# Performance work log

Measured on AMD Instinct MI355X. Metric: run time of the kernel, lower is better.

Reference implementation:

```python
import jax, jax.numpy as jnp
import numpy as np

B, S, D, H, FF = 4, 2048, 512, 8, 2048
HD = D // H
WINDOW = 64  # local attention half-window in rank space
EPS = 1e-5


def _layer_norm(v, g, b):
    m = jnp.mean(v, axis=-1, keepdims=True)
    var = jnp.mean(jnp.square(v - m), axis=-1, keepdims=True)
    return (v - m) / jnp.sqrt(var + EPS) * g + b


def setup_inputs() -> dict:
    key = jax.random.key(0)
    ks = jax.random.split(key, 10)
    sc = 0.02
    x = jax.random.normal(ks[0], (B, S, D), jnp.float32)
    padding_mask = jnp.zeros((B, S), dtype=bool)
    i = jnp.arange(S)
    local = jnp.abs(i[:, None] - i[None, :]) <= WINDOW
    glob = (i[:, None] == 0) | (i[None, :] == 0)  # global spectrum token at pos 0
    attn_mask = jnp.where(local | glob, 0.0, -jnp.inf).astype(jnp.float32)
    return {
        "x": x,
        "padding_mask": padding_mask,
        "attn_mask": attn_mask,
        "in_proj_w": jax.random.normal(ks[1], (3 * D, D), jnp.float32) * sc,
        "in_proj_b": jnp.zeros((3 * D,), jnp.float32),
        "out_proj_w": jax.random.normal(ks[2], (D, D), jnp.float32) * sc,
        "out_proj_b": jnp.zeros((D,), jnp.float32),
        "ln1_g": jnp.ones((D,), jnp.float32),
        "ln1_b": jnp.zeros((D,), jnp.float32),
        "ln2_g": jnp.ones((D,), jnp.float32),
        "ln2_b": jnp.zeros((D,), jnp.float32),
        "ff_w1": jax.random.normal(ks[3], (FF, D), jnp.float32) * sc,
        "ff_b1": jnp.zeros((FF,), jnp.float32),
        "ff_w2": jax.random.normal(ks[4], (D, FF), jnp.float32) * sc,
        "ff_b2": jnp.zeros((D,), jnp.float32),
    }


def reference(x, padding_mask, attn_mask, in_proj_w, in_proj_b, out_proj_w,
              out_proj_b, ln1_g, ln1_b, ln2_g, ln2_b, ff_w1, ff_b1, ff_w2, ff_b2):
    # pre-LN attention
    a = _layer_norm(x, ln1_g, ln1_b)
    qkv = a @ in_proj_w.T + in_proj_b  # [B,S,3D]
    q, k, v = jnp.split(qkv, 3, axis=-1)
    to_heads = lambda t: t.reshape(B, S, H, HD).transpose(0, 2, 1, 3)
    q, k, v = to_heads(q), to_heads(k), to_heads(v)
    scores = jnp.einsum('bhqd,bhkd->bhqk', q, k) * (HD ** -0.5)
    # float attn_mask path: key_padding_mask converted to additive -inf floats
    kpm = jnp.where(padding_mask, -jnp.inf, 0.0).astype(scores.dtype)
    scores = scores + attn_mask[None, None, :, :] + kpm[:, None, None, :]
    p = jax.nn.softmax(scores, axis=-1)
    o = jnp.einsum('bhqk,bhkd->bhqd', p, v).transpose(0, 2, 1, 3).reshape(B, S, D)
    o = o @ out_proj_w.T + out_proj_b
    x = x + o  # residual (dropout = 0)
    # pre-LN feed-forward with exact GELU (torch nn.GELU default)
    f = _layer_norm(x, ln2_g, ln2_b)
    f = jax.nn.gelu(f @ ff_w1.T + ff_b1, approximate=False) @ ff_w2.T + ff_b2
    return x + f
```

## Files before the change

### kernel.cpp

```cpp
#include <hip/hip_runtime.h>
#include <hip/hip_bf16.h>
#include <math.h>

namespace {

constexpr int kB = 4, kS = 2048, kD = 512, kH = 8, kFF = 2048;
constexpr int kM = kB * kS;
constexpr int kHD = kD / kH;
constexpr int kWin = 64;

typedef __attribute__((ext_vector_type(8))) short short8;
typedef __attribute__((ext_vector_type(4))) float f32x4;

__device__ __forceinline__ float bf2f(__hip_bfloat16 v) { return __bfloat162float(v); }
__device__ __forceinline__ __hip_bfloat16 f2bf(float v) { return __float2bfloat16(v); }
__device__ __forceinline__ int iclamp(int v, int lo, int hi) { return v < lo ? lo : (v > hi ? hi : v); }

__device__ __forceinline__ void async16(const void* g, void* l) {
  __builtin_amdgcn_global_load_lds((const __attribute__((address_space(1))) void*)g,
                                   (__attribute__((address_space(3))) void*)l, 16, 0, 0);
}

__device__ __forceinline__ void ln_one_row_f32(const float* xr, const float* g,
                                               const float* bta, __hip_bfloat16* outr, int lane) {
  int c = lane * 8;
  float4 v0 = *(const float4*)(xr + c);
  float4 v1 = *(const float4*)(xr + c + 4);
  float s  = v0.x + v0.y + v0.z + v0.w + v1.x + v1.y + v1.z + v1.w;
  float ss = v0.x*v0.x + v0.y*v0.y + v0.z*v0.z + v0.w*v0.w
           + v1.x*v1.x + v1.y*v1.y + v1.z*v1.z + v1.w*v1.w;
#pragma unroll
  for (int o = 32; o > 0; o >>= 1) { s += __shfl_xor(s, o); ss += __shfl_xor(ss, o); }
  float mean = s * (1.0f / kD);
  float inv  = rsqrtf(ss * (1.0f / kD) - mean * mean + 1e-5f);
  float4 g0 = *(const float4*)(g + c),   g1 = *(const float4*)(g + c + 4);
  float4 b0 = *(const float4*)(bta + c), b1 = *(const float4*)(bta + c + 4);
  union { __hip_bfloat16 h[8]; int4 u; } t;
  t.h[0] = f2bf((v0.x - mean) * inv * g0.x + b0.x);
  t.h[1] = f2bf((v0.y - mean) * inv * g0.y + b0.y);
  t.h[2] = f2bf((v0.z - mean) * inv * g0.z + b0.z);
  t.h[3] = f2bf((v0.w - mean) * inv * g0.w + b0.w);
  t.h[4] = f2bf((v1.x - mean) * inv * g1.x + b1.x);
  t.h[5] = f2bf((v1.y - mean) * inv * g1.y + b1.y);
  t.h[6] = f2bf((v1.z - mean) * inv * g1.z + b1.z);
  t.h[7] = f2bf((v1.w - mean) * inv * g1.w + b1.w);
  *(int4*)(outr + c) = t.u;
}

__global__ __launch_bounds__(256)
void prep(const float* __restrict__ iw, const float* __restrict__ ow,
          const float* __restrict__ f1, const float* __restrict__ f2,
          __hip_bfloat16* __restrict__ wq, __hip_bfloat16* __restrict__ wo,
          __hip_bfloat16* __restrict__ w1, __hip_bfloat16* __restrict__ w2,
          const float* __restrict__ x, const float* __restrict__ g,
          const float* __restrict__ bta, __hip_bfloat16* __restrict__ a) {
  const int id = blockIdx.x;
  if (id < 3072) {
    const float* s; __hip_bfloat16* d; int base;
    if (id < 768)       { s = iw; d = wq; base = id; }
    else if (id < 1024) { s = ow; d = wo; base = id - 768; }
    else if (id < 2048) { s = f1; d = w1; base = id - 1024; }
    else                { s = f2; d = w2; base = id - 2048; }
    int i = base * 1024 + threadIdx.x * 4;
    float4 v = *(const float4*)(s + i);
    union { __hip_bfloat16 h[4]; uint2 u; } t;
    t.h[0] = f2bf(v.x); t.h[1] = f2bf(v.y); t.h[2] = f2bf(v.z); t.h[3] = f2bf(v.w);
    *(uint2*)(d + i) = t.u;
  } else {
    int row = (id - 3072) * 4 + (threadIdx.x >> 6);
    ln_one_row_f32(x + (size_t)row * kD, g, bta, a + (size_t)row * kD, threadIdx.x & 63);
  }
}

__global__ __launch_bounds__(256)
void ln_rows_bf(const __hip_bfloat16* __restrict__ x, const float* __restrict__ g,
                const float* __restrict__ bta, __hip_bfloat16* __restrict__ out) {
  int row = blockIdx.x * 4 + (threadIdx.x >> 6);
  int lane = threadIdx.x & 63;
  int c = lane * 8;
  union { short8 v; __hip_bfloat16 hh[8]; } u;
  u.v = *(const short8*)(x + (size_t)row * kD + c);
  float f[8];
  float s = 0.f, ss = 0.f;
#pragma unroll
  for (int i = 0; i < 8; ++i) { f[i] = bf2f(u.hh[i]); s += f[i]; ss += f[i] * f[i]; }
#pragma unroll
  for (int o = 32; o > 0; o >>= 1) { s += __shfl_xor(s, o); ss += __shfl_xor(ss, o); }
  float mean = s * (1.0f / kD);
  float inv  = rsqrtf(ss * (1.0f / kD) - mean * mean + 1e-5f);
  float4 g0 = *(const float4*)(g + c),   g1 = *(const float4*)(g + c + 4);
  float4 b0 = *(const float4*)(bta + c), b1 = *(const float4*)(bta + c + 4);
  union { __hip_bfloat16 h[8]; int4 v; } t;
  t.h[0] = f2bf((f[0] - mean) * inv * g0.x + b0.x);
  t.h[1] = f2bf((f[1] - mean) * inv * g0.y + b0.y);
  t.h[2] = f2bf((f[2] - mean) * inv * g0.z + b0.z);
  t.h[3] = f2bf((f[3] - mean) * inv * g0.w + b0.w);
  t.h[4] = f2bf((f[4] - mean) * inv * g1.x + b1.x);
  t.h[5] = f2bf((f[5] - mean) * inv * g1.y + b1.y);
  t.h[6] = f2bf((f[6] - mean) * inv * g1.z + b1.z);
  t.h[7] = f2bf((f[7] - mean) * inv * g1.w + b1.w);
  *(int4*)(out + (size_t)row * kD + c) = t.v;
}

__global__ __launch_bounds__(64)
void attn_tile(const __hip_bfloat16* __restrict__ qkv, const __hip_bfloat16* __restrict__ vt,
               __hip_bfloat16* __restrict__ o) {
  const int bh = blockIdx.x;
  const int tq = blockIdx.y;
  const int b = bh >> 3, h = bh & 7;
  const int lane = threadIdx.x;
  const int quad = lane >> 4, col = lane & 15;
  const int q0 = tq * 16;
  const int kbase = q0 - kWin;

  __shared__ __hip_bfloat16 Pt[160 * 20];

  const __hip_bfloat16* base = qkv + (size_t)b * kS * (3 * kD);
  const __hip_bfloat16* vt_bh = vt + (size_t)(b * kH + h) * kHD * kS;

  short8 aq0, aq1;
  {
    const __hip_bfloat16* qrow = base + (size_t)(q0 + col) * (3 * kD) + h * kHD + quad * 8;
    aq0 = *(const short8*)qrow;
    aq1 = *(const short8*)(qrow + 32);
  }

  f32x4 sc[10];
#pragma unroll
  for (int t = 0; t < 10; ++t) {
    int krow = (t < 9) ? iclamp(kbase + t * 16 + col, 0, kS - 1) : col;
    const short8* kp = (const short8*)(base + (size_t)krow * (3 * kD) + kD + h * kHD + quad * 8);
    f32x4 a = (f32x4){0.f, 0.f, 0.f, 0.f};
    a = __builtin_amdgcn_mfma_f32_16x16x32_bf16(aq0, kp[0], a, 0, 0, 0);
    a = __builtin_amdgcn_mfma_f32_16x16x32_bf16(aq1, kp[4], a, 0, 0, 0);
    sc[t] = a;
  }

  float rowmax[4] = {-1e30f, -1e30f, -1e30f, -1e30f};
#pragma unroll
  for (int t = 0; t < 10; ++t) {
#pragma unroll
    for (int r = 0; r < 4; ++r) {
      int q = q0 + quad * 4 + r;
      bool valid;
      if (t < 9) {
        int k = kbase + t * 16 + col;
        valid = (k >= 0) && (k < kS) && ((q - k <= kWin && k - q <= kWin) || k == 0);
      } else {
        valid = (col == 0) && (kbase > 0);
      }
      float s = valid ? sc[t][r] * 0.125f : -1e30f;
      sc[t][r] = s;
      rowmax[r] = fmaxf(rowmax[r], s);
    }
  }
#pragma unroll
  for (int r = 0; r < 4; ++r)
#pragma unroll
    for (int off = 1; off < 16; off <<= 1)
      rowmax[r] = fmaxf(rowmax[r], __shfl_xor(rowmax[r], off));

  float rowsum[4] = {0.f, 0.f, 0.f, 0.f};
#pragma unroll
  for (int t = 0; t < 10; ++t)
#pragma unroll
    for (int r = 0; r < 4; ++r) {
      float e = __expf(sc[t][r] - rowmax[r]);
      sc[t][r] = e;
      rowsum[r] += e;
    }
#pragma unroll
  for (int r = 0; r < 4; ++r)
#pragma unroll
    for (int off = 1; off < 16; off <<= 1)
      rowsum[r] += __shfl_xor(rowsum[r], off);

#pragma unroll
  for (int t = 0; t < 10; ++t) {
    union { ushort u[4]; unsigned long long ll; } pk;
#pragma unroll
    for (int r = 0; r < 4; ++r) {
      __hip_bfloat16 hv = f2bf(sc[t][r]);
      pk.u[r] = *(ushort*)&hv;
    }
    *(unsigned long long*)&Pt[(t * 16 + col) * 20 + quad * 4] = pk.ll;
  }
  __syncthreads();

  f32x4 oacc[4];
#pragma unroll
  for (int n = 0; n < 4; ++n) oacc[n] = (f32x4){0.f, 0.f, 0.f, 0.f};

#pragma unroll
  for (int c = 0; c < 5; ++c) {
    union { short s[8]; short8 v; } pa;
#pragma unroll
    for (int j = 0; j < 8; ++j) pa.s[j] = *(const short*)&Pt[(c * 32 + quad * 8 + j) * 20 + col];
    const int kc = c * 32 + quad * 8;
    const int kstart = (kc < 144) ? iclamp(kbase + kc, 0, kS - 8) : (kc - 144);
#pragma unroll
    for (int n = 0; n < 4; ++n) {
      short8 vb = *(const short8*)(vt_bh + (size_t)(n * 16 + col) * kS + kstart);
      oacc[n] = __builtin_amdgcn_mfma_f32_16x16x32_bf16(pa.v, vb, oacc[n], 0, 0, 0);
    }
  }

#pragma unroll
  for (int n = 0; n < 4; ++n)
#pragma unroll
    for (int r = 0; r < 4; ++r) {
      int q = q0 + quad * 4 + r;
      o[(size_t)(b * kS + q) * kD + h * kHD + n * 16 + col] = f2bf(oacc[n][r] / rowsum[r]);
    }
}

__global__ __launch_bounds__(1024)
void attn_q0(const __hip_bfloat16* __restrict__ qkv, const __hip_bfloat16* __restrict__ vt,
             __hip_bfloat16* __restrict__ o) {
  const int b = blockIdx.x >> 3, h = blockIdx.x & 7;
  const int t = threadIdx.x;
  const int lane = t & 63, wid = t >> 6;
  __shared__ float qs[kHD];
  __shared__ float sc[kS];
  __shared__ float redm[16];
  __shared__ float reds[16];
  __shared__ float part[16][kHD];

  const __hip_bfloat16* base = qkv + (size_t)b * kS * (3 * kD);
  const __hip_bfloat16* vt_bh = vt + (size_t)(b * kH + h) * kHD * kS;
  if (t < kHD) qs[t] = bf2f(base[h * kHD + t]) * 0.125f;
  __syncthreads();

  float m = -1e30f;
#pragma unroll
  for (int it = 0; it < 2; ++it) {
    int k = t + it * 1024;
    const short8* kp = (const short8*)(base + (size_t)k * (3 * kD) + kD + h * kHD);
    float s = 0.f;
#pragma unroll
    for (int cc = 0; cc < 8; ++cc) {
      union { short8 v; __hip_bfloat16 hh[8]; } u;
      u.v = kp[cc];
#pragma unroll
      for (int d = 0; d < 8; ++d) s += qs[cc * 8 + d] * bf2f(u.hh[d]);
    }
    sc[k] = s;
    m = fmaxf(m, s);
  }
#pragma unroll
  for (int off = 32; off > 0; off >>= 1) m = fmaxf(m, __shfl_xor(m, off));
  if (lane == 0) redm[wid] = m;
  __syncthreads();
  float M = redm[0];
#pragma unroll
  for (int i = 1; i < 16; ++i) M = fmaxf(M, redm[i]);

  float ls = 0.f;
#pragma unroll
  for (int it = 0; it < 2; ++it) {
    int k = t + it * 1024;
    float e = __expf(sc[k] - M);
    sc[k] = e;
    ls += e;
  }
#pragma unroll
  for (int off = 32; off > 0; off >>= 1) ls += __shfl_xor(ls, off);
  if (lane == 0) reds[wid] = ls;
  __syncthreads();
  float L = 0.f;
#pragma unroll
  for (int i = 0; i < 16; ++i) L += reds[i];

  float a = 0.f;
  const int d = lane;
  const __hip_bfloat16* vr = vt_bh + (size_t)d * kS + wid * 128;
#pragma unroll
  for (int c = 0; c < 16; ++c) {
    union { short8 v; __hip_bfloat16 hh[8]; } u;
    u.v = *(const short8*)(vr + c * 8);
#pragma unroll
    for (int j = 0; j < 8; ++j) a += sc[wid * 128 + c * 8 + j] * bf2f(u.hh[j]);
  }
  part[wid][d] = a;
  __syncthreads();
  if (t < kHD) {
    float s = 0.f;
#pragma unroll
    for (int c = 0; c < 16; ++c) s += part[c][t];
    o[(size_t)(b * kS) * kD + h * kHD + t] = f2bf(s / L);
  }
}

template <int TN, int NB, int EPI, int WVT, typename OT, typename RT>
__global__ __launch_bounds__(256, (TN == 64) ? 4 : 4)
void gemm_bt(const __hip_bfloat16* __restrict__ A, const __hip_bfloat16* __restrict__ W,
             const float* __restrict__ bias, const RT* __restrict__ resid,
             OT* __restrict__ C, __hip_bfloat16* __restrict__ vt, int Ndim, int K) {
  constexpr int NF = TN / 32;
  __shared__ __hip_bfloat16 As[128 * 64];
  __shared__ __hip_bfloat16 Ws[TN * 64];

  const int id = blockIdx.x;
  const int rr = id & 7, tt = id >> 3;
  const int nb = tt % NB, mb = (tt / NB) * 8 + rr;

  const int tid = threadIdx.x;
  const int lane = tid & 63, w = tid >> 6;
  const int wm = w >> 1, wn = w & 1;
  const int quad = lane >> 4, mrow = lane & 15;
  const int m0 = mb * 128, n0 = nb * TN;

  const int lrow = lane >> 3;
  const int lcol = ((lane & 7) ^ lrow) << 3;

  f32x4 acc[4][NF];
#pragma unroll
  for (int i = 0; i < 4; ++i)
#pragma unroll
    for (int j = 0; j < NF; ++j) acc[i][j] = (f32x4){0.f, 0.f, 0.f, 0.f};

  for (int kt = 0; kt < K; kt += 64) {
#pragma unroll
    for (int it = 0; it < 4; ++it) {
      int c = w * 4 + it;
      async16(A + (size_t)(m0 + c * 8 + lrow) * K + kt + lcol, &As[c * 512]);
    }
#pragma unroll
    for (int it = 0; it < NF; ++it) {
      int c = w * NF + it;
      async16(W + (size_t)(n0 + c * 8 + lrow) * K + kt + lcol, &Ws[c * 512]);
    }
    __syncthreads();
#pragma unroll
    for (int kk = 0; kk < 64; kk += 32) {
      const int ch = (kk >> 3) + quad;
      const int sw = (ch ^ (mrow & 7)) << 3;
      short8 af[4], wf[NF];
#pragma unroll
      for (int i = 0; i < 4; ++i)
        af[i] = *(const short8*)&As[(wm * 64 + i * 16 + mrow) * 64 + sw];
#pragma unroll
      for (int j = 0; j < NF; ++j)
        wf[j] = *(const short8*)&Ws[(wn * (TN / 2) + j * 16 + mrow) * 64 + sw];
#pragma unroll
      for (int i = 0; i < 4; ++i)
#pragma unroll
        for (int j = 0; j < NF; ++j)
          acc[i][j] = __builtin_amdgcn_mfma_f32_16x16x32_bf16(af[i], wf[j], acc[i][j], 0, 0, 0);
    }
    __syncthreads();
  }

  if (WVT && n0 >= 1024) {
#pragma unroll
    for (int i = 0; i < 4; ++i) {
      int row0 = m0 + wm * 64 + i * 16 + quad * 4;
      int bb = row0 >> 11, ss = row0 & 2047;
#pragma unroll
      for (int j = 0; j < NF; ++j) {
        int colv = n0 + wn * (TN / 2) + j * 16 + mrow - 1024;
        int hh = colv >> 6, dd = colv & 63;
        float bsv = bias[1024 + colv];
        union { __hip_bfloat16 h[4]; unsigned long long u; } pk;
#pragma unroll
        for (int r = 0; r < 4; ++r) pk.h[r] = f2bf(acc[i][j][r] + bsv);
        *(unsigned long long*)(vt + ((size_t)(bb * kH + hh) * kHD + dd) * kS + ss) = pk.u;
      }
    }
    return;
  }

#pragma unroll
  for (int i = 0; i < 4; ++i) {
#pragma unroll
    for (int r = 0; r < 4; ++r) {
      int row = m0 + wm * 64 + i * 16 + quad * 4 + r;
#pragma unroll
      for (int j = 0; j < NF; ++j) {
        int col = n0 + wn * (TN / 2) + j * 16 + mrow;
        float v = acc[i][j][r] + bias[col];
        if (EPI == 1) v = 0.5f * v * (1.0f + erff(v * 0.70710678118f));
        if (EPI == 2) v += ((const float*)resid)[(size_t)row * Ndim + col];
        if (EPI == 3) v += bf2f(((const __hip_bfloat16*)resid)[(size_t)row * Ndim + col]);
        if constexpr (__is_same(OT, float)) C[(size_t)row * Ndim + col] = v;
        else                                C[(size_t)row * Ndim + col] = f2bf(v);
      }
    }
  }
}

}

extern "C" void kernel_launch(void* const* d_in, const int* in_sizes, int n_in,
                              void* d_out, int out_size, void* d_ws, size_t ws_size,
                              hipStream_t stream) {
  const float* x          = (const float*)d_in[0];
  const float* in_proj_w  = (const float*)d_in[3];
  const float* in_proj_b  = (const float*)d_in[4];
  const float* out_proj_w = (const float*)d_in[5];
  const float* out_proj_b = (const float*)d_in[6];
  const float* ln1_g      = (const float*)d_in[7];
  const float* ln1_b      = (const float*)d_in[8];
  const float* ln2_g      = (const float*)d_in[9];
  const float* ln2_b      = (const float*)d_in[10];
  const float* ff_w1      = (const float*)d_in[11];
  const float* ff_b1      = (const float*)d_in[12];
  const float* ff_w2      = (const float*)d_in[13];
  const float* ff_b2      = (const float*)d_in[14];
  float* out = (float*)d_out;

  char* ws = (char*)d_ws;
  size_t off = 0;
  auto carve = [&](size_t bytes) { char* p = ws + off; off += (bytes + 255) & ~(size_t)255; return p; };
  __hip_bfloat16* wqkv_bf = (__hip_bfloat16*)carve((size_t)3 * kD * kD * 2);
  __hip_bfloat16* wout_bf = (__hip_bfloat16*)carve((size_t)kD * kD * 2);
  __hip_bfloat16* wff1_bf = (__hip_bfloat16*)carve((size_t)kFF * kD * 2);
  __hip_bfloat16* wff2_bf = (__hip_bfloat16*)carve((size_t)kD * kFF * 2);
  __hip_bfloat16* a_bf    = (__hip_bfloat16*)carve((size_t)kM * kD * 2);
  __hip_bfloat16* qkv_bf  = (__hip_bfloat16*)carve((size_t)kM * 3 * kD * 2);
  __hip_bfloat16* vt      = (__hip_bfloat16*)carve((size_t)kM * kD * 2);
  __hip_bfloat16* o_bf    = (__hip_bfloat16*)carve((size_t)kM * kD * 2);
  __hip_bfloat16* r1b     = (__hip_bfloat16*)carve((size_t)kM * kD * 2);
  __hip_bfloat16* ln2_bf  = (__hip_bfloat16*)carve((size_t)kM * kD * 2);
  __hip_bfloat16* ff1_bf  = (__hip_bfloat16*)carve((size_t)kM * kFF * 2);

  prep<<<5120, 256, 0, stream>>>(in_proj_w, out_proj_w, ff_w1, ff_w2,
                                 wqkv_bf, wout_bf, wff1_bf, wff2_bf,
                                 x, ln1_g, ln1_b, a_bf);
  gemm_bt<128, 12, 0, 1, __hip_bfloat16, float><<<64 * 12, 256, 0, stream>>>(
      a_bf, wqkv_bf, in_proj_b, nullptr, qkv_bf, vt, 3 * kD, kD);
  attn_tile<<<dim3(kB * kH, kS / 16), 64, 0, stream>>>(qkv_bf, vt, o_bf);
  attn_q0<<<kB * kH, 1024, 0, stream>>>(qkv_bf, vt, o_bf);
  gemm_bt<64, 8, 2, 0, __hip_bfloat16, float><<<64 * 8, 256, 0, stream>>>(
      o_bf, wout_bf, out_proj_b, x, r1b, nullptr, kD, kD);
  ln_rows_bf<<<kM / 4, 256, 0, stream>>>(r1b, ln2_g, ln2_b, ln2_bf);
  gemm_bt<128, 16, 1, 0, __hip_bfloat16, float><<<64 * 16, 256, 0, stream>>>(
      ln2_bf, wff1_bf, ff_b1, nullptr, ff1_bf, nullptr, kFF, kD);
  gemm_bt<64, 8, 3, 0, float, __hip_bfloat16><<<64 * 8, 256, 0, stream>>>(
      ff1_bf, wff2_bf, ff_b2, r1b, out, nullptr, kD, kFF);
}
```

Baseline: 250.5 us.

## Merge global-token attention into tile kernel, stage V-transpose through LDS, use bf16 residual

The separate attn_q0 launch is removed. Its query-0 full-row attention now runs as an extra blockIdx.y==0 block of attn_tile, using a single 64-thread wave that loops over all 2048 keys. The V-transpose epilogue of the QKV GEMM now stages tiles in swizzled LDS and writes 16-byte rows, replacing scattered 8-byte stores. The prep kernel also writes a bf16 copy of x so the out-proj residual reads half the bytes. The cost is extra prep writes, a slow serial global-row block that can stretch the attention tail, and a less precise residual.

```diff
diff --git a/kernel.cpp b/kernel.cpp
--- a/kernel.cpp
+++ b/kernel.cpp
@@ -19,32 +19,6 @@
 __device__ __forceinline__ void async16(const void* g, void* l) {
   __builtin_amdgcn_global_load_lds((const __attribute__((address_space(1))) void*)g,
                                    (__attribute__((address_space(3))) void*)l, 16, 0, 0);
-}
-
-__device__ __forceinline__ void ln_one_row_f32(const float* xr, const float* g,
-                                               const float* bta, __hip_bfloat16* outr, int lane) {
-  int c = lane * 8;
-  float4 v0 = *(const float4*)(xr + c);
-  float4 v1 = *(const float4*)(xr + c + 4);
-  float s  = v0.x + v0.y + v0.z + v0.w + v1.x + v1.y + v1.z + v1.w;
-  float ss = v0.x*v0.x + v0.y*v0.y + v0.z*v0.z + v0.w*v0.w
-           + v1.x*v1.x + v1.y*v1.y + v1.z*v1.z + v1.w*v1.w;
-#pragma unroll
-  for (int o = 32; o > 0; o >>= 1) { s += __shfl_xor(s, o); ss += __shfl_xor(ss, o); }
-  float mean = s * (1.0f / kD);
-  float inv  = rsqrtf(ss * (1.0f / kD) - mean * mean + 1e-5f);
-  float4 g0 = *(const float4*)(g + c),   g1 = *(const float4*)(g + c + 4);
-  float4 b0 = *(const float4*)(bta + c), b1 = *(const float4*)(bta + c + 4);
-  union { __hip_bfloat16 h[8]; int4 u; } t;
-  t.h[0] = f2bf((v0.x - mean) * inv * g0.x + b0.x);
-  t.h[1] = f2bf((v0.y - mean) * inv * g0.y + b0.y);
-  t.h[2] = f2bf((v0.z - mean) * inv * g0.z + b0.z);
-  t.h[3] = f2bf((v0.w - mean) * inv * g0.w + b0.w);
-  t.h[4] = f2bf((v1.x - mean) * inv * g1.x + b1.x);
-  t.h[5] = f2bf((v1.y - mean) * inv * g1.y + b1.y);
-  t.h[6] = f2bf((v1.z - mean) * inv * g1.z + b1.z);
-  t.h[7] = f2bf((v1.w - mean) * inv * g1.w + b1.w);
-  *(int4*)(outr + c) = t.u;
 }
 
 __global__ __launch_bounds__(256)
@@ -53,7 +27,8 @@
           __hip_bfloat16* __restrict__ wq, __hip_bfloat16* __restrict__ wo,
           __hip_bfloat16* __restrict__ w1, __hip_bfloat16* __restrict__ w2,
           const float* __restrict__ x, const float* __restrict__ g,
-          const float* __restrict__ bta, __hip_bfloat16* __restrict__ a) {
+          const float* __restrict__ bta, __hip_bfloat16* __restrict__ a,
+          __hip_bfloat16* __restrict__ xb) {
   const int id = blockIdx.x;
   if (id < 3072) {
     const float* s; __hip_bfloat16* d; int base;
@@ -68,7 +43,34 @@
     *(uint2*)(d + i) = t.u;
   } else {
     int row = (id - 3072) * 4 + (threadIdx.x >> 6);
-    ln_one_row_f32(x + (size_t)row * kD, g, bta, a + (size_t)row * kD, threadIdx.x & 63);
+    int lane = threadIdx.x & 63;
+    const float* xr = x + (size_t)row * kD;
+    int c = lane * 8;
+    float4 v0 = *(const float4*)(xr + c);
+    float4 v1 = *(const float4*)(xr + c + 4);
+    union { __hip_bfloat16 h[8]; int4 u; } xr8;
+    xr8.h[0] = f2bf(v0.x); xr8.h[1] = f2bf(v0.y); xr8.h[2] = f2bf(v0.z); xr8.h[3] = f2bf(v0.w);
+    xr8.h[4] = f2bf(v1.x); xr8.h[5] = f2bf(v1.y); xr8.h[6] = f2bf(v1.z); xr8.h[7] = f2bf(v1.w);
+    *(int4*)(xb + (size_t)row * kD + c) = xr8.u;
+    float s  = v0.x + v0.y + v0.z + v0.w + v1.x + v1.y + v1.z + v1.w;
+    float ss = v0.x*v0.x + v0.y*v0.y + v0.z*v0.z + v0.w*v0.w
+             + v1.x*v1.x + v1.y*v1.y + v1.z*v1.z + v1.w*v1.w;
+#pragma unroll
+    for (int o = 32; o > 0; o >>= 1) { s += __shfl_xor(s, o); ss += __shfl_xor(ss, o); }
+    float mean = s * (1.0f / kD);
+    float inv  = rsqrtf(ss * (1.0f / kD) - mean * mean + 1e-5f);
+    float4 g0 = *(const float4*)(g + c),   g1 = *(const float4*)(g + c + 4);
+    float4 b0 = *(const float4*)(bta + c), b1 = *(const float4*)(bta + c + 4);
+    union { __hip_bfloat16 h[8]; int4 u; } t;
+    t.h[0] = f2bf((v0.x - mean) * inv * g0.x + b0.x);
+    t.h[1] = f2bf((v0.y - mean) * inv * g0.y + b0.y);
+    t.h[2] = f2bf((v0.z - mean) * inv * g0.z + b0.z);
+    t.h[3] = f2bf((v0.w - mean) * inv * g0.w + b0.w);
+    t.h[4] = f2bf((v1.x - mean) * inv * g1.x + b1.x);
+    t.h[5] = f2bf((v1.y - mean) * inv * g1.y + b1.y);
+    t.h[6] = f2bf((v1.z - mean) * inv * g1.z + b1.z);
+    t.h[7] = f2bf((v1.w - mean) * inv * g1.w + b1.w);
+    *(int4*)(a + (size_t)row * kD + c) = t.u;
   }
 }
 
@@ -106,17 +108,61 @@
 void attn_tile(const __hip_bfloat16* __restrict__ qkv, const __hip_bfloat16* __restrict__ vt,
                __hip_bfloat16* __restrict__ o) {
   const int bh = blockIdx.x;
-  const int tq = blockIdx.y;
   const int b = bh >> 3, h = bh & 7;
   const int lane = threadIdx.x;
+
+  __shared__ float smem_f[2048];
+  __shared__ float qs0[kHD];
+  __hip_bfloat16* Pt = (__hip_bfloat16*)smem_f;
+
+  const __hip_bfloat16* base = qkv + (size_t)b * kS * (3 * kD);
+  const __hip_bfloat16* vt_bh = vt + (size_t)(b * kH + h) * kHD * kS;
+
+  if (blockIdx.y == 0) {
+    qs0[lane] = bf2f(base[h * kHD + lane]) * 0.125f;
+    __syncthreads();
+    float m = -1e30f;
+    for (int kk = lane; kk < kS; kk += 64) {
+      const short8* kp = (const short8*)(base + (size_t)kk * (3 * kD) + kD + h * kHD);
+      float s = 0.f;
+#pragma unroll
+      for (int cc = 0; cc < 8; ++cc) {
+        union { short8 v; __hip_bfloat16 hh[8]; } u;
+        u.v = kp[cc];
+#pragma unroll
+        for (int d = 0; d < 8; ++d) s += qs0[cc * 8 + d] * bf2f(u.hh[d]);
+      }
+      smem_f[kk] = s;
+      m = fmaxf(m, s);
+    }
+#pragma unroll
+    for (int off = 32; off > 0; off >>= 1) m = fmaxf(m, __shfl_xor(m, off));
+    float ls = 0.f;
+    __syncthreads();
+    for (int kk = lane; kk < kS; kk += 64) {
+      float e = __expf(smem_f[kk] - m);
+      smem_f[kk] = e;
+      ls += e;
+    }
+#pragma unroll
+    for (int off = 32; off > 0; off >>= 1) ls += __shfl_xor(ls, off);
+    __syncthreads();
+    float a = 0.f;
+    const __hip_bfloat16* vr = vt_bh + (size_t)lane * kS;
+    for (int c = 0; c < kS / 8; ++c) {
+      union { short8 v; __hip_bfloat16 hh[8]; } u;
+      u.v = *(const short8*)(vr + c * 8);
+#pragma unroll
+      for (int j = 0; j < 8; ++j) a += smem_f[c * 8 + j] * bf2f(u.hh[j]);
+    }
+    o[(size_t)(b * kS) * kD + h * kHD + lane] = f2bf(a / ls);
+    return;
+  }
+
+  const int tq = blockIdx.y - 1;
   const int quad = lane >> 4, col = lane & 15;
   const int q0 = tq * 16;
   const int kbase = q0 - kWin;
-
-  __shared__ __hip_bfloat16 Pt[160 * 20];
-
-  const __hip_bfloat16* base = qkv + (size_t)b * kS * (3 * kD);
-  const __hip_bfloat16* vt_bh = vt + (size_t)(b * kH + h) * kHD * kS;
 
   short8 aq0, aq1;
   {
@@ -210,89 +256,13 @@
 #pragma unroll
     for (int r = 0; r < 4; ++r) {
       int q = q0 + quad * 4 + r;
+      if (q == 0) continue;
       o[(size_t)(b * kS + q) * kD + h * kHD + n * 16 + col] = f2bf(oacc[n][r] / rowsum[r]);
     }
 }
 
-__global__ __launch_bounds__(1024)
-void attn_q0(const __hip_bfloat16* __restrict__ qkv, const __hip_bfloat16* __restrict__ vt,
-             __hip_bfloat16* __restrict__ o) {
-  const int b = blockIdx.x >> 3, h = blockIdx.x & 7;
-  const int t = threadIdx.x;
-  const int lane = t & 63, wid = t >> 6;
-  __shared__ float qs[kHD];
-  __shared__ float sc[kS];
-  __shared__ float redm[16];
-  __shared__ float reds[16];
-  __shared__ float part[16][kHD];
-
-  const __hip_bfloat16* base = qkv + (size_t)b * kS * (3 * kD);
-  const __hip_bfloat16* vt_bh = vt + (size_t)(b * kH + h) * kHD * kS;
-  if (t < kHD) qs[t] = bf2f(base[h * kHD + t]) * 0.125f;
-  __syncthreads();
-
-  float m = -1e30f;
-#pragma unroll
-  for (int it = 0; it < 2; ++it) {
-    int k = t + it * 1024;
-    const short8* kp = (const short8*)(base + (size_t)k * (3 * kD) + kD + h * kHD);
-    float s = 0.f;
-#pragma unroll
-    for (int cc = 0; cc < 8; ++cc) {
-      union { short8 v; __hip_bfloat16 hh[8]; } u;
-      u.v = kp[cc];
-#pragma unroll
-      for (int d = 0; d < 8; ++d) s += qs[cc * 8 + d] * bf2f(u.hh[d]);
-    }
-    sc[k] = s;
-    m = fmaxf(m, s);
-  }
-#pragma unroll
-  for (int off = 32; off > 0; off >>= 1) m = fmaxf(m, __shfl_xor(m, off));
-  if (lane == 0) redm[wid] = m;
-  __syncthreads();
-  float M = redm[0];
-#pragma unroll
-  for (int i = 1; i < 16; ++i) M = fmaxf(M, redm[i]);
-
-  float ls = 0.f;
-#pragma unroll
-  for (int it = 0; it < 2; ++it) {
-    int k = t + it * 1024;
-    float e = __expf(sc[k] - M);
-    sc[k] = e;
-    ls += e;
-  }
-#pragma unroll
-  for (int off = 32; off > 0; off >>= 1) ls += __shfl_xor(ls, off);
-  if (lane == 0) reds[wid] = ls;
-  __syncthreads();
-  float L = 0.f;
-#pragma unroll
-  for (int i = 0; i < 16; ++i) L += reds[i];
-
-  float a = 0.f;
-  const int d = lane;
-  const __hip_bfloat16* vr = vt_bh + (size_t)d * kS + wid * 128;
-#pragma unroll
-  for (int c = 0; c < 16; ++c) {
-    union { short8 v; __hip_bfloat16 hh[8]; } u;
-    u.v = *(const short8*)(vr + c * 8);
-#pragma unroll
-    for (int j = 0; j < 8; ++j) a += sc[wid * 128 + c * 8 + j] * bf2f(u.hh[j]);
-  }
-  part[wid][d] = a;
-  __syncthreads();
-  if (t < kHD) {
-    float s = 0.f;
-#pragma unroll
-    for (int c = 0; c < 16; ++c) s += part[c][t];
-    o[(size_t)(b * kS) * kD + h * kHD + t] = f2bf(s / L);
-  }
-}
-
 template <int TN, int NB, int EPI, int WVT, typename OT, typename RT>
-__global__ __launch_bounds__(256, (TN == 64) ? 4 : 4)
+__global__ __launch_bounds__(256, 4)
 void gemm_bt(const __hip_bfloat16* __restrict__ A, const __hip_bfloat16* __restrict__ W,
              const float* __restrict__ bias, const RT* __restrict__ resid,
              OT* __restrict__ C, __hip_bfloat16* __restrict__ vt, int Ndim, int K) {
@@ -351,23 +321,42 @@
     __syncthreads();
   }
 
-  if (WVT && n0 >= 1024) {
-#pragma unroll
-    for (int i = 0; i < 4; ++i) {
-      int row0 = m0 + wm * 64 + i * 16 + quad * 4;
-      int bb = row0 >> 11, ss = row0 & 2047;
-#pragma unroll
-      for (int j = 0; j < NF; ++j) {
-        int colv = n0 + wn * (TN / 2) + j * 16 + mrow - 1024;
-        int hh = colv >> 6, dd = colv & 63;
-        float bsv = bias[1024 + colv];
-        union { __hip_bfloat16 h[4]; unsigned long long u; } pk;
-#pragma unroll
-        for (int r = 0; r < 4; ++r) pk.h[r] = f2bf(acc[i][j][r] + bsv);
-        *(unsigned long long*)(vt + ((size_t)(bb * kH + hh) * kHD + dd) * kS + ss) = pk.u;
+  if constexpr (WVT) {
+    if (n0 >= 1024) {
+      __hip_bfloat16* Ls = As;
+      const int bb = m0 >> 11, ss0 = m0 & (kS - 1);
+      const int n0v = n0 - 1024;
+#pragma unroll
+      for (int p = 0; p < 2; ++p) {
+        __syncthreads();
+#pragma unroll
+        for (int jj = 0; jj < 2; ++jj) {
+          int j = p * 2 + jj;
+          int lr = wn * 32 + jj * 16 + mrow;
+          float bs = bias[1024 + n0v + wn * 64 + j * 16 + mrow];
+#pragma unroll
+          for (int i = 0; i < 4; ++i) {
+            int tok = wm * 64 + i * 16 + quad * 4;
+            int tw = tok ^ ((lr & 15) << 3);
+            union { __hip_bfloat16 h[4]; unsigned long long u; } pk;
+#pragma unroll
+            for (int r = 0; r < 4; ++r) pk.h[r] = f2bf(acc[i][j][r] + bs);
+            *(unsigned long long*)&Ls[lr * 128 + tw] = pk.u;
+          }
+        }
+        __syncthreads();
+#pragma unroll
+        for (int i2 = 0; i2 < 4; ++i2) {
+          int c = i2 * 256 + tid;
+          int lr = c >> 4, off = (c & 15) << 3;
+          int tw = off ^ ((lr & 15) << 3);
+          short8 v = *(const short8*)&Ls[lr * 128 + tw];
+          int colv = (lr >> 5) * 64 + p * 32 + (lr & 31);
+          *(short8*)(vt + (size_t)(bb * 512 + n0v + colv) * kS + ss0 + off) = v;
+        }
       }
-    }
-    return;
+      return;
+    }
   }
 
 #pragma unroll
@@ -380,7 +369,6 @@
         int col = n0 + wn * (TN / 2) + j * 16 + mrow;
         float v = acc[i][j][r] + bias[col];
         if (EPI == 1) v = 0.5f * v * (1.0f + erff(v * 0.70710678118f));
-        if (EPI == 2) v += ((const float*)resid)[(size_t)row * Ndim + col];
         if (EPI == 3) v += bf2f(((const __hip_bfloat16*)resid)[(size_t)row * Ndim + col]);
         if constexpr (__is_same(OT, float)) C[(size_t)row * Ndim + col] = v;
         else                                C[(size_t)row * Ndim + col] = f2bf(v);
@@ -417,6 +405,7 @@
   __hip_bfloat16* wff1_bf = (__hip_bfloat16*)carve((size_t)kFF * kD * 2);
   __hip_bfloat16* wff2_bf = (__hip_bfloat16*)carve((size_t)kD * kFF * 2);
   __hip_bfloat16* a_bf    = (__hip_bfloat16*)carve((size_t)kM * kD * 2);
+  __hip_bfloat16* x_bf    = (__hip_bfloat16*)carve((size_t)kM * kD * 2);
   __hip_bfloat16* qkv_bf  = (__hip_bfloat16*)carve((size_t)kM * 3 * kD * 2);
   __hip_bfloat16* vt      = (__hip_bfloat16*)carve((size_t)kM * kD * 2);
   __hip_bfloat16* o_bf    = (__hip_bfloat16*)carve((size_t)kM * kD * 2);
@@ -426,13 +415,12 @@
 
   prep<<<5120, 256, 0, stream>>>(in_proj_w, out_proj_w, ff_w1, ff_w2,
                                  wqkv_bf, wout_bf, wff1_bf, wff2_bf,
-                                 x, ln1_g, ln1_b, a_bf);
+                                 x, ln1_g, ln1_b, a_bf, x_bf);
   gemm_bt<128, 12, 0, 1, __hip_bfloat16, float><<<64 * 12, 256, 0, stream>>>(
       a_bf, wqkv_bf, in_proj_b, nullptr, qkv_bf, vt, 3 * kD, kD);
-  attn_tile<<<dim3(kB * kH, kS / 16), 64, 0, stream>>>(qkv_bf, vt, o_bf);
-  attn_q0<<<kB * kH, 1024, 0, stream>>>(qkv_bf, vt, o_bf);
-  gemm_bt<64, 8, 2, 0, __hip_bfloat16, float><<<64 * 8, 256, 0, stream>>>(
-      o_bf, wout_bf, out_proj_b, x, r1b, nullptr, kD, kD);
+  attn_tile<<<dim3(kB * kH, kS / 16 + 1), 64, 0, stream>>>(qkv_bf, vt, o_bf);
+  gemm_bt<64, 8, 3, 0, __hip_bfloat16, __hip_bfloat16><<<64 * 8, 256, 0, stream>>>(
+      o_bf, wout_bf, out_proj_b, x_bf, r1b, nullptr, kD, kD);
   ln_rows_bf<<<kM / 4, 256, 0, stream>>>(r1b, ln2_g, ln2_b, ln2_bf);
   gemm_bt<128, 16, 1, 0, __hip_bfloat16, float><<<64 * 16, 256, 0, stream>>>(
       ln2_bf, wff1_bf, ff_b1, nullptr, ff1_bf, nullptr, kFF, kD);
```

Result: slower. 266.7 us (+6.5%).

## Pack attention tiles per block, stage V-transpose via LDS, use bf16 residual

Applied to the files above, without the earlier changes.

Several unrelated changes land together. The attention kernel now runs four 16-query tiles per 256-thread block, each wave with its own LDS slice. The V-transpose epilogue of the QKV GEMM is staged through swizzled LDS so it can issue coalesced 16-byte stores instead of scattered 8-byte writes. The prep kernel also writes a bf16 copy of x, so the out-projection residual reads bf16 instead of fp32, at the cost of residual precision and an extra write. The attention kernel additionally skips the write for query 0, which is handled by attn_q0.

```diff
diff --git a/kernel.cpp b/kernel.cpp
--- a/kernel.cpp
+++ b/kernel.cpp
@@ -19,32 +19,6 @@
 __device__ __forceinline__ void async16(const void* g, void* l) {
   __builtin_amdgcn_global_load_lds((const __attribute__((address_space(1))) void*)g,
                                    (__attribute__((address_space(3))) void*)l, 16, 0, 0);
-}
-
-__device__ __forceinline__ void ln_one_row_f32(const float* xr, const float* g,
-                                               const float* bta, __hip_bfloat16* outr, int lane) {
-  int c = lane * 8;
-  float4 v0 = *(const float4*)(xr + c);
-  float4 v1 = *(const float4*)(xr + c + 4);
-  float s  = v0.x + v0.y + v0.z + v0.w + v1.x + v1.y + v1.z + v1.w;
-  float ss = v0.x*v0.x + v0.y*v0.y + v0.z*v0.z + v0.w*v0.w
-           + v1.x*v1.x + v1.y*v1.y + v1.z*v1.z + v1.w*v1.w;
-#pragma unroll
-  for (int o = 32; o > 0; o >>= 1) { s += __shfl_xor(s, o); ss += __shfl_xor(ss, o); }
-  float mean = s * (1.0f / kD);
-  float inv  = rsqrtf(ss * (1.0f / kD) - mean * mean + 1e-5f);
-  float4 g0 = *(const float4*)(g + c),   g1 = *(const float4*)(g + c + 4);
-  float4 b0 = *(const float4*)(bta + c), b1 = *(const float4*)(bta + c + 4);
-  union { __hip_bfloat16 h[8]; int4 u; } t;
-  t.h[0] = f2bf((v0.x - mean) * inv * g0.x + b0.x);
-  t.h[1] = f2bf((v0.y - mean) * inv * g0.y + b0.y);
-  t.h[2] = f2bf((v0.z - mean) * inv * g0.z + b0.z);
-  t.h[3] = f2bf((v0.w - mean) * inv * g0.w + b0.w);
-  t.h[4] = f2bf((v1.x - mean) * inv * g1.x + b1.x);
-  t.h[5] = f2bf((v1.y - mean) * inv * g1.y + b1.y);
-  t.h[6] = f2bf((v1.z - mean) * inv * g1.z + b1.z);
-  t.h[7] = f2bf((v1.w - mean) * inv * g1.w + b1.w);
-  *(int4*)(outr + c) = t.u;
 }
 
 __global__ __launch_bounds__(256)
@@ -53,7 +27,8 @@
           __hip_bfloat16* __restrict__ wq, __hip_bfloat16* __restrict__ wo,
           __hip_bfloat16* __restrict__ w1, __hip_bfloat16* __restrict__ w2,
           const float* __restrict__ x, const float* __restrict__ g,
-          const float* __restrict__ bta, __hip_bfloat16* __restrict__ a) {
+          const float* __restrict__ bta, __hip_bfloat16* __restrict__ a,
+          __hip_bfloat16* __restrict__ xb) {
   const int id = blockIdx.x;
   if (id < 3072) {
     const float* s; __hip_bfloat16* d; int base;
@@ -68,7 +43,34 @@
     *(uint2*)(d + i) = t.u;
   } else {
     int row = (id - 3072) * 4 + (threadIdx.x >> 6);
-    ln_one_row_f32(x + (size_t)row * kD, g, bta, a + (size_t)row * kD, threadIdx.x & 63);
+    int lane = threadIdx.x & 63;
+    const float* xr = x + (size_t)row * kD;
+    int c = lane * 8;
+    float4 v0 = *(const float4*)(xr + c);
+    float4 v1 = *(const float4*)(xr + c + 4);
+    union { __hip_bfloat16 h[8]; int4 u; } xr8;
+    xr8.h[0] = f2bf(v0.x); xr8.h[1] = f2bf(v0.y); xr8.h[2] = f2bf(v0.z); xr8.h[3] = f2bf(v0.w);
+    xr8.h[4] = f2bf(v1.x); xr8.h[5] = f2bf(v1.y); xr8.h[6] = f2bf(v1.z); xr8.h[7] = f2bf(v1.w);
+    *(int4*)(xb + (size_t)row * kD + c) = xr8.u;
+    float s  = v0.x + v0.y + v0.z + v0.w + v1.x + v1.y + v1.z + v1.w;
+    float ss = v0.x*v0.x + v0.y*v0.y + v0.z*v0.z + v0.w*v0.w
+             + v1.x*v1.x + v1.y*v1.y + v1.z*v1.z + v1.w*v1.w;
+#pragma unroll
+    for (int o = 32; o > 0; o >>= 1) { s += __shfl_xor(s, o); ss += __shfl_xor(ss, o); }
+    float mean = s * (1.0f / kD);
+    float inv  = rsqrtf(ss * (1.0f / kD) - mean * mean + 1e-5f);
+    float4 g0 = *(const float4*)(g + c),   g1 = *(const float4*)(g + c + 4);
+    float4 b0 = *(const float4*)(bta + c), b1 = *(const float4*)(bta + c + 4);
+    union { __hip_bfloat16 h[8]; int4 u; } t;
+    t.h[0] = f2bf((v0.x - mean) * inv * g0.x + b0.x);
+    t.h[1] = f2bf((v0.y - mean) * inv * g0.y + b0.y);
+    t.h[2] = f2bf((v0.z - mean) * inv * g0.z + b0.z);
+    t.h[3] = f2bf((v0.w - mean) * inv * g0.w + b0.w);
+    t.h[4] = f2bf((v1.x - mean) * inv * g1.x + b1.x);
+    t.h[5] = f2bf((v1.y - mean) * inv * g1.y + b1.y);
+    t.h[6] = f2bf((v1.z - mean) * inv * g1.z + b1.z);
+    t.h[7] = f2bf((v1.w - mean) * inv * g1.w + b1.w);
+    *(int4*)(a + (size_t)row * kD + c) = t.u;
   }
 }
 
@@ -102,18 +104,20 @@
   *(int4*)(out + (size_t)row * kD + c) = t.v;
 }
 
-__global__ __launch_bounds__(64)
+__global__ __launch_bounds__(256)
 void attn_tile(const __hip_bfloat16* __restrict__ qkv, const __hip_bfloat16* __restrict__ vt,
                __hip_bfloat16* __restrict__ o) {
   const int bh = blockIdx.x;
-  const int tq = blockIdx.y;
   const int b = bh >> 3, h = bh & 7;
-  const int lane = threadIdx.x;
+  const int tid = threadIdx.x;
+  const int lane = tid & 63, w = tid >> 6;
+  const int tq = blockIdx.y * 4 + w;
   const int quad = lane >> 4, col = lane & 15;
   const int q0 = tq * 16;
   const int kbase = q0 - kWin;
 
-  __shared__ __hip_bfloat16 Pt[160 * 20];
+  __shared__ __hip_bfloat16 PtAll[4 * 160 * 20];
+  __hip_bfloat16* Pt = PtAll + w * 160 * 20;
 
   const __hip_bfloat16* base = qkv + (size_t)b * kS * (3 * kD);
   const __hip_bfloat16* vt_bh = vt + (size_t)(b * kH + h) * kHD * kS;
@@ -185,7 +189,6 @@
     }
     *(unsigned long long*)&Pt[(t * 16 + col) * 20 + quad * 4] = pk.ll;
   }
-  __syncthreads();
 
   f32x4 oacc[4];
 #pragma unroll
@@ -210,6 +213,7 @@
 #pragma unroll
     for (int r = 0; r < 4; ++r) {
       int q = q0 + quad * 4 + r;
+      if (q == 0) continue;
       o[(size_t)(b * kS + q) * kD + h * kHD + n * 16 + col] = f2bf(oacc[n][r] / rowsum[r]);
     }
 }
@@ -292,7 +296,7 @@
 }
 
 template <int TN, int NB, int EPI, int WVT, typename OT, typename RT>
-__global__ __launch_bounds__(256, (TN == 64) ? 4 : 4)
+__global__ __launch_bounds__(256, 4)
 void gemm_bt(const __hip_bfloat16* __restrict__ A, const __hip_bfloat16* __restrict__ W,
              const float* __restrict__ bias, const RT* __restrict__ resid,
              OT* __restrict__ C, __hip_bfloat16* __restrict__ vt, int Ndim, int K) {
@@ -351,23 +355,42 @@
     __syncthreads();
   }
 
-  if (WVT && n0 >= 1024) {
-#pragma unroll
-    for (int i = 0; i < 4; ++i) {
-      int row0 = m0 + wm * 64 + i * 16 + quad * 4;
-      int bb = row0 >> 11, ss = row0 & 2047;
-#pragma unroll
-      for (int j = 0; j < NF; ++j) {
-        int colv = n0 + wn * (TN / 2) + j * 16 + mrow - 1024;
-        int hh = colv >> 6, dd = colv & 63;
-        float bsv = bias[1024 + colv];
-        union { __hip_bfloat16 h[4]; unsigned long long u; } pk;
-#pragma unroll
-        for (int r = 0; r < 4; ++r) pk.h[r] = f2bf(acc[i][j][r] + bsv);
-        *(unsigned long long*)(vt + ((size_t)(bb * kH + hh) * kHD + dd) * kS + ss) = pk.u;
+  if constexpr (WVT) {
+    if (n0 >= 1024) {
+      __hip_bfloat16* Ls = As;
+      const int bb = m0 >> 11, ss0 = m0 & (kS - 1);
+      const int n0v = n0 - 1024;
+#pragma unroll
+      for (int p = 0; p < 2; ++p) {
+        __syncthreads();
+#pragma unroll
+        for (int jj = 0; jj < 2; ++jj) {
+          int j = p * 2 + jj;
+          int lr = wn * 32 + jj * 16 + mrow;
+          float bs = bias[1024 + n0v + wn * 64 + j * 16 + mrow];
+#pragma unroll
+          for (int i = 0; i < 4; ++i) {
+            int tok = wm * 64 + i * 16 + quad * 4;
+            int tw = tok ^ ((lr & 15) << 3);
+            union { __hip_bfloat16 h[4]; unsigned long long u; } pk;
+#pragma unroll
+            for (int r = 0; r < 4; ++r) pk.h[r] = f2bf(acc[i][j][r] + bs);
+            *(unsigned long long*)&Ls[lr * 128 + tw] = pk.u;
+          }
+        }
+        __syncthreads();
+#pragma unroll
+        for (int i2 = 0; i2 < 4; ++i2) {
+          int c = i2 * 256 + tid;
+          int lr = c >> 4, off = (c & 15) << 3;
+          int tw = off ^ ((lr & 15) << 3);
+          short8 v = *(const short8*)&Ls[lr * 128 + tw];
+          int colv = (lr >> 5) * 64 + p * 32 + (lr & 31);
+          *(short8*)(vt + (size_t)(bb * 512 + n0v + colv) * kS + ss0 + off) = v;
+        }
       }
-    }
-    return;
+      return;
+    }
   }
 
 #pragma unroll
@@ -380,7 +403,6 @@
         int col = n0 + wn * (TN / 2) + j * 16 + mrow;
         float v = acc[i][j][r] + bias[col];
         if (EPI == 1) v = 0.5f * v * (1.0f + erff(v * 0.70710678118f));
-        if (EPI == 2) v += ((const float*)resid)[(size_t)row * Ndim + col];
         if (EPI == 3) v += bf2f(((const __hip_bfloat16*)resid)[(size_t)row * Ndim + col]);
         if constexpr (__is_same(OT, float)) C[(size_t)row * Ndim + col] = v;
         else                                C[(size_t)row * Ndim + col] = f2bf(v);
@@ -417,6 +439,7 @@
   __hip_bfloat16* wff1_bf = (__hip_bfloat16*)carve((size_t)kFF * kD * 2);
   __hip_bfloat16* wff2_bf = (__hip_bfloat16*)carve((size_t)kD * kFF * 2);
   __hip_bfloat16* a_bf    = (__hip_bfloat16*)carve((size_t)kM * kD * 2);
+  __hip_bfloat16* x_bf    = (__hip_bfloat16*)carve((size_t)kM * kD * 2);
   __hip_bfloat16* qkv_bf  = (__hip_bfloat16*)carve((size_t)kM * 3 * kD * 2);
   __hip_bfloat16* vt      = (__hip_bfloat16*)carve((size_t)kM * kD * 2);
   __hip_bfloat16* o_bf    = (__hip_bfloat16*)carve((size_t)kM * kD * 2);
@@ -426,13 +449,13 @@
 
   prep<<<5120, 256, 0, stream>>>(in_proj_w, out_proj_w, ff_w1, ff_w2,
                                  wqkv_bf, wout_bf, wff1_bf, wff2_bf,
-                                 x, ln1_g, ln1_b, a_bf);
+                                 x, ln1_g, ln1_b, a_bf, x_bf);
   gemm_bt<128, 12, 0, 1, __hip_bfloat16, float><<<64 * 12, 256, 0, stream>>>(
       a_bf, wqkv_bf, in_proj_b, nullptr, qkv_bf, vt, 3 * kD, kD);
-  attn_tile<<<dim3(kB * kH, kS / 16), 64, 0, stream>>>(qkv_bf, vt, o_bf);
+  attn_tile<<<dim3(kB * kH, kS / 64), 256, 0, stream>>>(qkv_bf, vt, o_bf);
   attn_q0<<<kB * kH, 1024, 0, stream>>>(qkv_bf, vt, o_bf);
-  gemm_bt<64, 8, 2, 0, __hip_bfloat16, float><<<64 * 8, 256, 0, stream>>>(
-      o_bf, wout_bf, out_proj_b, x, r1b, nullptr, kD, kD);
+  gemm_bt<64, 8, 3, 0, __hip_bfloat16, __hip_bfloat16><<<64 * 8, 256, 0, stream>>>(
+      o_bf, wout_bf, out_proj_b, x_bf, r1b, nullptr, kD, kD);
   ln_rows_bf<<<kM / 4, 256, 0, stream>>>(r1b, ln2_g, ln2_b, ln2_bf);
   gemm_bt<128, 16, 1, 0, __hip_bfloat16, float><<<64 * 16, 256, 0, stream>>>(
       ln2_bf, wff1_bf, ff_b1, nullptr, ff1_bf, nullptr, kFF, kD);
```

New measurement: 242.1 us. 3.4% less time.
